# Kernel tuning notes

Measured on AMD Instinct MI355X. Metric: run time of the kernel, lower is better.

Reference implementation:

```python
import jax, jax.numpy as jnp
import numpy as np

# PyTorch bicubic (a=-0.75), half-pixel coords, scale factor 2 -> fixed fractional
# offset t=0.5 for every output pixel, giving constant taps at src offsets [-1,0,1,2].
CUBIC_W = np.array([-0.09375, 0.59375, 0.59375, -0.09375], dtype=np.float32)


def _down_last(x):
    """Bicubic 2x downsample along the last axis (PyTorch semantics, border clamp)."""
    n = x.shape[-1]
    no = n // 2
    idx = jnp.clip(2 * jnp.arange(no)[:, None] + jnp.arange(-1, 3)[None, :], 0, n - 1)  # (no,4)
    g = x[..., idx]  # (..., no, 4)
    return jnp.einsum('...ok,k->...o', g, jnp.asarray(CUBIC_W, dtype=x.dtype))


def _downsample_bicubic(x):
    # separable: width then height (order irrelevant)
    x = _down_last(x)
    x = jnp.swapaxes(x, -1, -2)
    x = _down_last(x)
    return jnp.swapaxes(x, -1, -2)


def _fftpack_hilbert(x):
    """scipy.fftpack.hilbert: y_j = 1j*sign(j)*x_j in Fourier space, Nyquist zeroed."""
    n = x.shape[0]
    X = np.fft.fft(x)
    sgn = np.zeros(n)
    sgn[1:n // 2] = 1.0
    sgn[n // 2 + 1:] = -1.0
    return np.real(np.fft.ifft(1j * sgn * X))


def _db8_filters():
    gl = np.array([-0.00011747678400228192, 0.0006754494059985568, -0.0003917403729959771,
                   -0.00487035299301066, 0.008746094047015655, 0.013981027917015516,
                   -0.04408825393106472, -0.01736930100202211, 0.128747426620186,
                   0.00047248457399797254, -0.2840155429624281, -0.015829105256023893,
                   0.5853546836548691, 0.6756307362980128, 0.3128715909144659,
                   0.05441584224308161])
    gh = np.array([-0.05441584224308161, 0.3128715909144659, -0.6756307362980128,
                   0.5853546836548691, 0.015829105256023893, -0.2840155429624281,
                   -0.00047248457399797254, 0.128747426620186, 0.01736930100202211,
                   -0.04408825393106472, -0.013981027917015516, 0.008746094047015655,
                   0.00487035299301066, -0.0003917403729959771, -0.0006754494059985568,
                   -0.00011747678400228192])
    fl = _fftpack_hilbert(gl)
    fh = _fftpack_hilbert(gh)
    return gl, gh, fl, fh


def setup_inputs() -> dict:
    key = jax.random.key(0)
    image = jax.random.normal(key, (4, 16, 512, 512), dtype=jnp.float32)
    gl, gh, fl, fh = _db8_filters()
    return {
        'image': image,
        'gl': jnp.asarray(gl, dtype=jnp.float32),
        'gh': jnp.asarray(gh, dtype=jnp.float32),
        'fl': jnp.asarray(fl, dtype=jnp.float32),
        'fh': jnp.asarray(fh, dtype=jnp.float32),
    }


def reference(image, gl, gh, fl, fh):
    # The original _column_convolve/_row_convolve never shift X (out += X*h[idx]),
    # so after the reflect-pad gather and centered slice, colfilter/rowfilter
    # reduce exactly to X * sum(h). Each sub-band is therefore
    # downsample(image) * sum(col_filter) * sum(row_filter).
    sg, sh = jnp.sum(gl), jnp.sum(gh)
    sfl, sfh = jnp.sum(fl), jnp.sum(fh)
    D = _downsample_bicubic(image)  # (B, C, H/2, W/2)
    LL = jnp.concatenate([D * (sg * sg), D * (sfl * sg), D * (sg * sfl), D * (sfl * sfl)], axis=1)
    b1 = jnp.concatenate([D * (sg * sh), D * (sfl * sh), D * (sg * sfh), D * (sfl * sfh)], axis=1)
    b2 = jnp.concatenate([D * (sh * sg), D * (sfh * sg), D * (sh * sfl), D * (sfh * sfl)], axis=1)
    b3 = jnp.concatenate([D * (sh * sh), D * (sfh * sh), D * (sh * sfh), D * (sfh * sfh)], axis=1)
    H = jnp.stack([b1, b2, b3], axis=2)  # (B, 4C, 3, H/2, W/2)
    return (LL, H)
```

## Files before the change

### kernel.cpp

```cpp
#include <hip/hip_runtime.h>

__global__ void qwt_sums_kernel(const float* __restrict__ gl, const float* __restrict__ gh,
                                const float* __restrict__ fl, const float* __restrict__ fh,
                                float* __restrict__ ws) {
    int t = threadIdx.x;
    if (t < 4) {
        const float* p = (t == 0) ? gl : (t == 1) ? gh : (t == 2) ? fl : fh;
        float s = 0.f;
        #pragma unroll
        for (int i = 0; i < 16; i++) s += p[i];
        ws[t] = s;
    }
}

__global__ __launch_bounds__(256) void qwt_main_kernel(const float* __restrict__ img,
                                                       const float* __restrict__ ws,
                                                       float* __restrict__ out) {
    const float w0 = -0.09375f, w1 = 0.59375f;

    int t    = blockIdx.x * 256 + threadIdx.x;
    int lane = t & 63;
    int row  = t >> 6;
    int y    = row & 255;
    int bc   = row >> 8;
    int x0   = lane << 2;

    float sg = ws[0], sh = ws[1], sfl = ws[2], sfh = ws[3];

    const float* src = img + (size_t)bc * (512 * 512);

    int cb = 2 * x0 - 1;
    int c[10];
    #pragma unroll
    for (int k = 0; k < 10; k++) {
        int cc = cb + k;
        cc = cc < 0 ? 0 : (cc > 511 ? 511 : cc);
        c[k] = cc;
    }

    float acc0 = 0.f, acc1 = 0.f, acc2 = 0.f, acc3 = 0.f;
    #pragma unroll
    for (int j = 0; j < 4; j++) {
        int ry = 2 * y - 1 + j;
        ry = ry < 0 ? 0 : (ry > 511 ? 511 : ry);
        const float* rp = src + (size_t)ry * 512;
        float r0 = rp[c[0]], r1 = rp[c[1]], r2 = rp[c[2]], r3 = rp[c[3]], r4 = rp[c[4]];
        float r5 = rp[c[5]], r6 = rp[c[6]], r7 = rp[c[7]], r8 = rp[c[8]], r9 = rp[c[9]];
        float wj = (j == 0 || j == 3) ? w0 : w1;
        float h0 = w0 * r0 + w1 * r1 + w1 * r2 + w0 * r3;
        float h1 = w0 * r2 + w1 * r3 + w1 * r4 + w0 * r5;
        float h2 = w0 * r4 + w1 * r5 + w1 * r6 + w0 * r7;
        float h3 = w0 * r6 + w1 * r7 + w1 * r8 + w0 * r9;
        acc0 += wj * h0; acc1 += wj * h1; acc2 += wj * h2; acc3 += wj * h3;
    }

    int b  = bc >> 4;
    int cc_ = bc & 15;
    size_t rowoff = ((size_t)y << 8) + (size_t)x0;
    const size_t P  = 65536;
    const size_t HB = 16777216;

    #pragma unroll
    for (int q = 0; q < 4; q++) {
        float f1g = (q & 1) ? sfl : sg;
        float f1h = (q & 1) ? sfh : sh;
        float f2g = (q & 2) ? sfl : sg;
        float f2h = (q & 2) ? sfh : sh;

        size_t chan = (size_t)(b * 64 + q * 16 + cc_);

        {
            float s = f1g * f2g;
            float4 v = make_float4(acc0 * s, acc1 * s, acc2 * s, acc3 * s);
            *(float4*)(out + chan * P + rowoff) = v;
        }
        size_t hbase = HB + chan * 3 * P + rowoff;
        {
            float s = f1g * f2h;
            float4 v = make_float4(acc0 * s, acc1 * s, acc2 * s, acc3 * s);
            *(float4*)(out + hbase) = v;
        }
        {
            float s = f1h * f2g;
            float4 v = make_float4(acc0 * s, acc1 * s, acc2 * s, acc3 * s);
            *(float4*)(out + hbase + P) = v;
        }
        {
            float s = f1h * f2h;
            float4 v = make_float4(acc0 * s, acc1 * s, acc2 * s, acc3 * s);
            *(float4*)(out + hbase + 2 * P) = v;
        }
    }
}

extern "C" void kernel_launch(void* const* d_in, const int* in_sizes, int n_in,
                              void* d_out, int out_size, void* d_ws, size_t ws_size,
                              hipStream_t stream) {
    const float* img = (const float*)d_in[0];
    const float* gl  = (const float*)d_in[1];
    const float* gh  = (const float*)d_in[2];
    const float* fl  = (const float*)d_in[3];
    const float* fh  = (const float*)d_in[4];
    float* out = (float*)d_out;
    float* ws  = (float*)d_ws;

    qwt_sums_kernel<<<1, 64, 0, stream>>>(gl, gh, fl, fh, ws);
    qwt_main_kernel<<<4096, 256, 0, stream>>>(img, ws, out);
}
```

Measured before the change: 319.7 us.

## Stage input rows in LDS with padded stride for bicubic downsample reuse

Each block now loads the 10 source rows needed for 4 output rows into shared memory with coalesced float4 loads, padded to avoid bank conflicts. Threads then read their 4x10 stencil from LDS instead of issuing scattered global loads. This targets redundant, uncoalesced global reads and the re-reading of overlapping rows by different output rows, at the cost of a barrier and about 21KB of LDS per block.

```diff
diff --git a/kernel.cpp b/kernel.cpp
--- a/kernel.cpp
+++ b/kernel.cpp
@@ -13,39 +13,57 @@
     }
 }
 
+#define LSTRIDE 528
+
 __global__ __launch_bounds__(256) void qwt_main_kernel(const float* __restrict__ img,
                                                        const float* __restrict__ ws,
                                                        float* __restrict__ out) {
+    __shared__ float lds[10 * LSTRIDE];
+
     const float w0 = -0.09375f, w1 = 0.59375f;
 
-    int t    = blockIdx.x * 256 + threadIdx.x;
-    int lane = t & 63;
-    int row  = t >> 6;
-    int y    = row & 255;
-    int bc   = row >> 8;
-    int x0   = lane << 2;
+    int tid = threadIdx.x;
+    int blk = blockIdx.x;
+    int bc  = blk >> 6;
+    int y0  = (blk & 63) << 2;
 
     float sg = ws[0], sh = ws[1], sfl = ws[2], sfh = ws[3];
 
     const float* src = img + (size_t)bc * (512 * 512);
+    int srow_base = 2 * y0 - 1;
 
-    int cb = 2 * x0 - 1;
-    int c[10];
+    #pragma unroll
+    for (int it = 0; it < 5; it++) {
+        int i   = it * 256 + tid;
+        int row = i >> 7;
+        int c4  = (i & 127) << 2;
+        int sr  = srow_base + row;
+        sr = sr < 0 ? 0 : (sr > 511 ? 511 : sr);
+        float4 v = *(const float4*)(src + (size_t)sr * 512 + c4);
+        float* d = lds + row * LSTRIDE + c4 + (c4 >> 5);
+        d[0] = v.x; d[1] = v.y; d[2] = v.z; d[3] = v.w;
+    }
+    __syncthreads();
+
+    int lane = tid & 63;
+    int w    = tid >> 6;
+    int y    = y0 + w;
+    int x0   = lane << 2;
+
+    int scol[10];
     #pragma unroll
     for (int k = 0; k < 10; k++) {
-        int cc = cb + k;
+        int cc = 2 * x0 - 1 + k;
         cc = cc < 0 ? 0 : (cc > 511 ? 511 : cc);
-        c[k] = cc;
+        scol[k] = cc + (cc >> 5);
     }
 
     float acc0 = 0.f, acc1 = 0.f, acc2 = 0.f, acc3 = 0.f;
     #pragma unroll
     for (int j = 0; j < 4; j++) {
-        int ry = 2 * y - 1 + j;
-        ry = ry < 0 ? 0 : (ry > 511 ? 511 : ry);
-        const float* rp = src + (size_t)ry * 512;
-        float r0 = rp[c[0]], r1 = rp[c[1]], r2 = rp[c[2]], r3 = rp[c[3]], r4 = rp[c[4]];
-        float r5 = rp[c[5]], r6 = rp[c[6]], r7 = rp[c[7]], r8 = rp[c[8]], r9 = rp[c[9]];
+        const float* rp = lds + (2 * w + j) * LSTRIDE;
+        float r0 = rp[scol[0]], r1 = rp[scol[1]], r2 = rp[scol[2]], r3 = rp[scol[3]], r4 = rp[scol[4]];
+        float r5 = rp[scol[5]], r6 = rp[scol[6]], r7 = rp[scol[7]], r8 = rp[scol[8]], r9 = rp[scol[9]];
         float wj = (j == 0 || j == 3) ? w0 : w1;
         float h0 = w0 * r0 + w1 * r1 + w1 * r2 + w0 * r3;
         float h1 = w0 * r2 + w1 * r3 + w1 * r4 + w0 * r5;
@@ -54,7 +72,7 @@
         acc0 += wj * h0; acc1 += wj * h1; acc2 += wj * h2; acc3 += wj * h3;
     }
 
-    int b  = bc >> 4;
+    int b   = bc >> 4;
     int cc_ = bc & 15;
     size_t rowoff = ((size_t)y << 8) + (size_t)x0;
     const size_t P  = 65536;
```

Result: no change. 322.0 us (+0.7%).
